# Optimization experiments

Hardware: AMD Instinct MI355X
Metric: run time of the kernel (lower is better)

The kernel has to match this reference:

```python
import math
import jax, jax.numpy as jnp
import numpy as np

HEAD = 8
D_HEAD = 32
D_MODEL = 256
N = 20000
E_LOCAL = 80000
E_BOND = 60000
E_GLOBAL = 400000
MAX_DEG = 32
MAX_DIST = 64


def segment_softmax(x, seg, num_segments):
    # softmax over entries sharing the same segment id (scatter_softmax)
    m = jax.ops.segment_max(x, seg, num_segments=num_segments)
    e = jnp.exp(x - m[seg])
    s = jax.ops.segment_sum(e, seg, num_segments=num_segments)
    return e / s[seg]


def setup_inputs() -> dict:
    key = jax.random.key(0)
    ks = jax.random.split(key, 16)
    s_in = 1.0 / math.sqrt(D_MODEL)
    s_out = 1.0 / math.sqrt(2 * D_MODEL)
    dist_emb = jax.random.normal(ks[7], (MAX_DIST + 1, D_MODEL), jnp.float32) * 0.02
    dist_emb = dist_emb.at[MAX_DIST].set(0.0)  # padding_idx
    return {
        "f_node": jax.random.normal(ks[0], (N, D_MODEL), jnp.float32),
        "f_bond": jax.random.normal(ks[1], (E_BOND, D_MODEL), jnp.float32),
        "deg_matrix": jax.random.randint(ks[2], (N,), 0, MAX_DEG + 1),
        "dist_matrix": jax.random.randint(ks[3], (E_GLOBAL,), 0, MAX_DIST + 1),
        "bond_idx": jax.random.randint(ks[4], (2, E_LOCAL), 0, N),
        "query_idx": jax.random.randint(ks[5], (E_GLOBAL,), 0, N),
        "key_idx": jax.random.randint(ks[6], (E_GLOBAL,), 0, N),
        "attention_bond_idx": jnp.arange(E_BOND),
        "deg_emb": jax.random.normal(ks[8], (MAX_DEG + 1, D_MODEL), jnp.float32) * 0.02,
        "dist_emb": dist_emb,
        "Wq_w": jax.random.normal(ks[9], (D_MODEL, 2 * D_MODEL), jnp.float32) * s_in,
        "Wq_b": jnp.zeros((2 * D_MODEL,), jnp.float32),
        "Wk_w": jax.random.normal(ks[10], (D_MODEL, 2 * D_MODEL), jnp.float32) * s_in,
        "Wk_b": jnp.zeros((2 * D_MODEL,), jnp.float32),
        "Wv_w": jax.random.normal(ks[11], (D_MODEL, 2 * D_MODEL), jnp.float32) * s_in,
        "Wv_b": jnp.zeros((2 * D_MODEL,), jnp.float32),
        "out_w": jax.random.normal(ks[12], (2 * D_MODEL, D_MODEL), jnp.float32) * s_out,
        "out_b": jnp.zeros((D_MODEL,), jnp.float32),
        "bond_emb_w": jax.random.normal(ks[13], (D_MODEL, 2 * D_MODEL), jnp.float32) * s_in,
        "bond_emb_b": jnp.zeros((2 * D_MODEL,), jnp.float32),
        "bond_update_w": jax.random.normal(ks[14], (2 * D_MODEL, D_MODEL), jnp.float32) * s_out,
        "bond_update_b": jnp.zeros((D_MODEL,), jnp.float32),
    }


def reference(f_node, f_bond, deg_matrix, dist_matrix, bond_idx, query_idx, key_idx,
              attention_bond_idx, deg_emb, dist_emb, Wq_w, Wq_b, Wk_w, Wk_b, Wv_w, Wv_b,
              out_w, out_b, bond_emb_w, bond_emb_b, bond_update_w, bond_update_b):
    scale = 1.0 / math.sqrt(D_HEAD)
    n = f_node.shape[0]
    e_bond = f_bond.shape[0]

    f_deg = deg_emb[deg_matrix].reshape(n, HEAD, D_HEAD)                  # [N,H,Dh]
    ab_vb = f_bond @ bond_emb_w + bond_emb_b                               # [Eb,2D]
    attention_bond, value_bond = jnp.split(ab_vb, 2, axis=-1)
    attention_bond = attention_bond.reshape(e_bond, HEAD, D_HEAD)
    value_bond = value_bond.reshape(e_bond, HEAD, D_HEAD)
    f_dist = dist_emb[dist_matrix].reshape(-1, HEAD, D_HEAD)               # [Eg,H,Dh]

    q = (f_node @ Wq_w + Wq_b).reshape(n, 2 * HEAD, D_HEAD)
    k = (f_node @ Wk_w + Wk_b).reshape(n, 2 * HEAD, D_HEAD)
    v = (f_node @ Wv_w + Wv_b).reshape(n, 2 * HEAD, D_HEAD)
    q_local, q_global = q[:, :HEAD], q[:, HEAD:]
    k_local, k_global = k[:, :HEAD], k[:, HEAD:]
    v_local, v_global = v[:, :HEAD], v[:, HEAD:]

    src, dst = bond_idx[0], bond_idx[1]
    # ---- local (bond) attention ----
    score_local = q_local[dst] * k_local[src]                              # [El,H,Dh]
    score_local = score_local.at[:e_bond].add(attention_bond)
    score_local = score_local.sum(-1) * scale                              # [El,H]
    score_local = segment_softmax(score_local, dst, n)
    local_out = v_local[src].at[:e_bond].add(value_bond)
    local_out = local_out * score_local[:, :, None]
    local_out = jax.ops.segment_sum(local_out, dst, num_segments=n)
    local_out = local_out.reshape(n, HEAD * D_HEAD)

    # ---- global (distance) attention ----
    kg = k_global + f_deg
    score_global = q_global[query_idx] * kg[key_idx]                       # [Eg,H,Dh]
    score_global = score_global.at[attention_bond_idx].add(attention_bond)
    score_global = (score_global + f_dist).sum(-1) * scale                 # [Eg,H]
    score_global = segment_softmax(score_global, query_idx, n)
    global_out = v_global[key_idx] * score_global[:, :, None]
    global_out = jax.ops.segment_sum(global_out, query_idx, num_segments=n)
    global_out = global_out.reshape(n, HEAD * D_HEAD)

    out = jnp.concatenate([local_out, global_out], axis=-1) @ out_w + out_b  # [N,D]
    bond_out = jnp.concatenate([f_bond, out[src[:e_bond]]], axis=-1)
    bond_out = bond_out @ bond_update_w + bond_update_b                      # [Eb,D]
    return out, bond_out
```

## Files before the change

### kernel.cpp

```cpp
#include <hip/hip_runtime.h>
#include <math.h>

typedef unsigned short u16;
typedef unsigned int u32;
typedef __attribute__((ext_vector_type(8))) short s16x8;
typedef __attribute__((ext_vector_type(4))) unsigned short u16x4;
typedef __attribute__((ext_vector_type(4))) float f32x4;

__device__ __forceinline__ float bf2f(u16 x) { return __uint_as_float(((u32)x) << 16); }
__device__ __forceinline__ u16 f2bf(float f) {
    u32 u = __float_as_uint(f);
    u32 r = u + 0x7fffu + ((u >> 16) & 1u);
    return (u16)(r >> 16);
}

__device__ __forceinline__ void gll16(const u16* g, u16* l) {
    __builtin_amdgcn_global_load_lds((const __attribute__((address_space(1))) void*)g,
                                     (__attribute__((address_space(3))) void*)l,
                                     16, 0, 0);
}

template <int MODE>
__global__ __launch_bounds__(256) void gemm128(
    const u16* __restrict__ Abf, const u16* __restrict__ A2b,
    const u16* __restrict__ BT, const float* __restrict__ bias,
    u16* __restrict__ Cb, float* __restrict__ Cf, u16* __restrict__ C2b,
    const float* __restrict__ auxemb, const int* __restrict__ auxidx,
    float* __restrict__ absum, int M, int N, int K)
{
    __shared__ u16 lsmem[2 * 16384];

    const int tid = threadIdx.x;
    const int wave = tid >> 6;
    const int lane = tid & 63;
    const int l15 = lane & 15;
    const int quad = lane >> 4;
    const int wr = wave >> 1, wc = wave & 1;

    const int gx = gridDim.x;
    const int nwg = gx * gridDim.y;
    int flat = blockIdx.y * gx + blockIdx.x;
    {
        const int q = nwg >> 3, r8 = nwg & 7;
        const int xcd = flat & 7, loc = flat >> 3;
        flat = (xcd < r8 ? xcd * (q + 1) : r8 * (q + 1) + (xcd - r8) * q) + loc;
    }
    const int tileRow = (flat / gx) * 128;
    const int tileCol = (flat % gx) * 128;

    const int srow = tid >> 3;
    const int ks = ((tid & 7) ^ (srow & 7)) * 8;

    const u16 *gA[4], *gB[4], *gA2[4];
#pragma unroll
    for (int j = 0; j < 4; j++) {
        const int ra = j * 32 + srow;
        const int pa = (MODE == 3) ? 256 : K;
        gA[j] = Abf + (size_t)(tileRow + ra) * pa + ks;
        gB[j] = BT + (size_t)(tileCol + ra) * K + ks;
        if (MODE == 3)
            gA2[j] = A2b + (size_t)auxidx[min(tileRow + ra, M - 1)] * 256 + ks;
        else
            gA2[j] = nullptr;
    }

#define STAGE(TK, BUF)                                                         \
    {                                                                          \
        u16* lb_ = lsmem + (BUF)*16384;                                        \
        const int kk_ = (TK)*64;                                               \
        _Pragma("unroll")                                                      \
        for (int j = 0; j < 4; j++) {                                          \
            const u16* sa;                                                     \
            if (MODE == 3) sa = (kk_ < 256) ? gA[j] + kk_ : gA2[j] + (kk_ - 256); \
            else sa = gA[j] + kk_;                                             \
            gll16(sa, lb_ + j * 2048 + tid * 8);                               \
            gll16(gB[j] + kk_, lb_ + 8192 + j * 2048 + tid * 8);               \
        }                                                                      \
    }

    f32x4 acc[4][4] = {};
    const int nt = K >> 6;

    STAGE(0, 0);
    STAGE(1, 1);

    for (int t = 0; t < nt; ++t) {
        if (t + 2 < nt) asm volatile("s_waitcnt vmcnt(8)" ::: "memory");
        else            asm volatile("s_waitcnt vmcnt(0)" ::: "memory");
        __builtin_amdgcn_s_barrier();
        __builtin_amdgcn_sched_barrier(0);

        const u16* lb = lsmem + (t & 1) * 16384;
#pragma unroll
        for (int kh = 0; kh < 2; kh++) {
            const int xk = ((quad + 4 * kh) ^ (l15 & 7)) * 8;
            s16x8 a[4], b[4];
#pragma unroll
            for (int mi = 0; mi < 4; mi++)
                a[mi] = *(const s16x8*)(lb + (wr * 64 + mi * 16 + l15) * 64 + xk);
#pragma unroll
            for (int ni = 0; ni < 4; ni++)
                b[ni] = *(const s16x8*)(lb + 8192 + (wc * 64 + ni * 16 + l15) * 64 + xk);
#pragma unroll
            for (int mi = 0; mi < 4; mi++)
#pragma unroll
                for (int ni = 0; ni < 4; ni++)
                    acc[mi][ni] = __builtin_amdgcn_mfma_f32_16x16x32_bf16(
                        a[mi], b[ni], acc[mi][ni], 0, 0, 0);
        }

        __builtin_amdgcn_sched_barrier(0);
        asm volatile("s_waitcnt lgkmcnt(0)" ::: "memory");
        __builtin_amdgcn_s_barrier();
        __builtin_amdgcn_sched_barrier(0);
        if (t + 2 < nt) STAGE(t + 2, t & 1);
    }
#undef STAGE

#pragma unroll
    for (int mi = 0; mi < 4; mi++) {
#pragma unroll
        for (int i = 0; i < 4; i++) {
            const int r = tileRow + wr * 64 + mi * 16 + quad * 4 + i;
            const bool rok = (r < M);
#pragma unroll
            for (int ni = 0; ni < 4; ni++) {
                const int c = tileCol + wc * 64 + ni * 16 + l15;
                float v = acc[mi][ni][i] + bias[c];
                if (MODE == 2) {
                    if (tileCol < 256) {
                        float s = v;
                        s += __shfl_xor(s, 1, 16);
                        s += __shfl_xor(s, 2, 16);
                        s += __shfl_xor(s, 4, 16);
                        s += __shfl_xor(s, 8, 16);
                        if (rok && l15 == 0) atomicAdd(&absum[r * 8 + (c >> 5)], s);
                    } else {
                        if (rok) Cb[(size_t)r * 256 + (c - 256)] = f2bf(v);
                    }
                } else if (MODE == 3) {
                    if (rok) Cf[(size_t)r * N + c] = v;
                } else if (MODE == 4) {
                    if (rok) {
                        Cf[(size_t)r * N + c] = v;
                        C2b[(size_t)r * N + c] = f2bf(v);
                    }
                } else {
                    const int which = c >> 9;
                    const int cc = c & 511;
                    if (which == 1 && cc >= 256)
                        v += auxemb[(size_t)auxidx[min(r, M - 1)] * 256 + (cc - 256)];
                    if (rok) Cb[((size_t)which * M + r) * 512 + cc] = f2bf(v);
                }
            }
        }
    }
}

__global__ __launch_bounds__(256) void prep_k(
    const float* __restrict__ Wq_w, const float* __restrict__ Wk_w,
    const float* __restrict__ Wv_w, const float* __restrict__ be_w,
    const float* __restrict__ out_w, const float* __restrict__ bu_w,
    u16* __restrict__ wT,
    const float* __restrict__ Wq_b, const float* __restrict__ Wk_b,
    const float* __restrict__ Wv_b, float* __restrict__ biasC,
    const float* __restrict__ dist_emb, float* __restrict__ distsum)
{
    const int b = blockIdx.x;
    if (b < 3072) {
        const int idx6 = b >> 9;
        const int r = ((b & 511) << 8) + threadIdx.x;
        const float* s = (idx6 == 0) ? Wq_w : (idx6 == 1) ? Wk_w
                       : (idx6 == 2) ? Wv_w : (idx6 == 3) ? be_w
                       : (idx6 == 4) ? out_w : bu_w;
        u16* dst = wT + (size_t)idx6 * 131072;
        if (idx6 < 4) {
            const int n = r >> 8, k = r & 255;
            dst[r] = f2bf(s[(size_t)k * 512 + n]);
        } else {
            const int n = r >> 9, k = r & 511;
            dst[r] = f2bf(s[(size_t)k * 256 + n]);
        }
    } else {
        const int u = (b - 3072) * 256 + threadIdx.x;
        if (u < 512) biasC[u] = Wq_b[u];
        else if (u < 1024) biasC[u] = Wk_b[u - 512];
        else if (u < 1536) biasC[u] = Wv_b[u - 1024];
        else if (u < 1536 + 520) {
            const float* p = dist_emb + (size_t)(u - 1536) * 32;
            float sm = 0.f;
#pragma unroll
            for (int j = 0; j < 32; j++) sm += p[j];
            distsum[u - 1536] = sm;
        }
    }
}

__global__ __launch_bounds__(256) void cvt2_k(
    const float* __restrict__ f_node, const float* __restrict__ f_bond,
    u16* __restrict__ fnb, u16* __restrict__ fbb,
    int N_, int MPN, int EB, int MPB)
{
    const int t = blockIdx.x * 256 + threadIdx.x;
    const int q1 = MPN * 64;
    const int q2 = MPB * 64;
    if (t < q1) {
        const int r = t >> 6;
        f32x4 v = {0.f, 0.f, 0.f, 0.f};
        if (r < N_) v = *(const f32x4*)(f_node + (size_t)t * 4);
        u16x4 o;
#pragma unroll
        for (int j = 0; j < 4; j++) o[j] = f2bf(v[j]);
        *(u16x4*)(fnb + (size_t)t * 4) = o;
    } else if (t < q1 + q2) {
        const int u = t - q1;
        const int r = u >> 6;
        f32x4 v = {0.f, 0.f, 0.f, 0.f};
        if (r < EB) v = *(const f32x4*)(f_bond + (size_t)u * 4);
        u16x4 o;
#pragma unroll
        for (int j = 0; j < 4; j++) o[j] = f2bf(v[j]);
        *(u16x4*)(fbb + (size_t)u * 4) = o;
    }
}

__global__ __launch_bounds__(256) void hist2_k(const int* __restrict__ bdst,
                                               const int* __restrict__ qidx,
                                               int* __restrict__ cnt,
                                               int N_, int EL, int EG)
{
    const int e = blockIdx.x * 256 + threadIdx.x;
    if (e < EL) atomicAdd(&cnt[bdst[e]], 1);
    else if (e < EL + EG) atomicAdd(&cnt[N_ + qidx[e - EL]], 1);
}

__global__ __launch_bounds__(1024) void scan2_k(
    const int* __restrict__ cnt_l, int* __restrict__ offs_l, int* __restrict__ cur_l,
    const int* __restrict__ cnt_g, int* __restrict__ offs_g, int* __restrict__ cur_g,
    int n)
{
    const int* cnt = blockIdx.x ? cnt_g : cnt_l;
    int* offs = blockIdx.x ? offs_g : offs_l;
    int* cursor = blockIdx.x ? cur_g : cur_l;
    __shared__ int part[1024];
    const int tid = threadIdx.x;
    const int per = (n + 1023) / 1024;
    int local[32];
    int s = 0;
    for (int j = 0; j < per; j++) {
        int idx = tid * per + j;
        int c = (idx < n) ? cnt[idx] : 0;
        local[j] = s;
        s += c;
    }
    part[tid] = s;
    __syncthreads();
    for (int st = 1; st < 1024; st <<= 1) {
        int v = (tid >= st) ? part[tid - st] : 0;
        __syncthreads();
        part[tid] += v;
        __syncthreads();
    }
    int pre = (tid == 0) ? 0 : part[tid - 1];
    for (int j = 0; j < per; j++) {
        int idx = tid * per + j;
        if (idx < n) { int o = pre + local[j]; offs[idx] = o; cursor[idx] = o; }
    }
    if (tid == 1023) offs[n] = part[1023];
}

__global__ __launch_bounds__(256) void scatter2_k(
    const int* __restrict__ bdst, const int* __restrict__ qidx,
    int* __restrict__ cur_l, int* __restrict__ cur_g,
    int* __restrict__ list_l, int* __restrict__ list_g, int EL, int EG)
{
    const int e = blockIdx.x * 256 + threadIdx.x;
    if (e < EL) {
        int pos = atomicAdd(&cur_l[bdst[e]], 1);
        list_l[pos] = e;
    } else if (e < EL + EG) {
        const int e2 = e - EL;
        int pos = atomicAdd(&cur_g[qidx[e2]], 1);
        list_g[pos] = e2;
    }
}

template <bool GLOB>
__device__ __forceinline__ void attn_half(
    const u16* __restrict__ qb, const u16* __restrict__ kb,
    const u16* __restrict__ vbuf, const u16* __restrict__ vb,
    const int* __restrict__ offs, const int* __restrict__ lst,
    const int* __restrict__ oth, const int* __restrict__ dist,
    const float* __restrict__ absum, const float* __restrict__ distsum,
    u16* __restrict__ out, int node, int EB, float scale)
{
    const int lane = threadIdx.x & 63;
    const int head = lane >> 3;
    const int cbase = (GLOB ? 256 : 0) + lane * 4;

    const u16x4 qv = *(const u16x4*)(qb + (size_t)node * 512 + cbase);
    const float q0 = bf2f(qv[0]), q1 = bf2f(qv[1]), q2 = bf2f(qv[2]), q3 = bf2f(qv[3]);

    const int s0 = offs[node], s1 = offs[node + 1];
    float a0 = 0.f, a1 = 0.f, a2 = 0.f, a3 = 0.f, den = 0.f;
    const u16x4 zv = {0, 0, 0, 0};

#define LOADS(S, IDX)                                                          \
    {                                                                          \
        e##S = __shfl(e_l, (IDX));                                             \
        const int src = __shfl(src_l, (IDX));                                  \
        kv##S = *(const u16x4*)(kb + (size_t)src * 512 + cbase);               \
        vv##S = *(const u16x4*)(vbuf + (size_t)src * 512 + cbase);             \
        ab##S = (e##S < EB) ? absum[e##S * 8 + head] : 0.f;                    \
        if (GLOB) {                                                            \
            const int d = __shfl(d_l, (IDX));                                  \
            ds##S = distsum[d * 8 + head];                                     \
        }                                                                      \
        if (!GLOB)                                                             \
            wv##S = (e##S < EB) ? *(const u16x4*)(vb + (size_t)e##S * 256 +    \
                                                  lane * 4)                    \
                                : zv;                                          \
    }

#define COMP(S)                                                                \
    {                                                                          \
        float t = q0 * bf2f(kv##S[0]) + q1 * bf2f(kv##S[1]) +                  \
                  q2 * bf2f(kv##S[2]) + q3 * bf2f(kv##S[3]);                   \
        t += __shfl_xor(t, 1);                                                 \
        t += __shfl_xor(t, 2);                                                 \
        t += __shfl_xor(t, 4);                                                 \
        t += ab##S;                                                            \
        if (GLOB) t += ds##S;                                                  \
        const float p = __expf(t * scale);                                     \
        den += p;                                                              \
        float v0 = bf2f(vv##S[0]), v1 = bf2f(vv##S[1]);                        \
        float v2 = bf2f(vv##S[2]), v3 = bf2f(vv##S[3]);                        \
        if (!GLOB) {                                                           \
            v0 += bf2f(wv##S[0]); v1 += bf2f(wv##S[1]);                        \
            v2 += bf2f(wv##S[2]); v3 += bf2f(wv##S[3]);                        \
        }                                                                      \
        a0 += p * v0; a1 += p * v1; a2 += p * v2; a3 += p * v3;                \
    }

    for (int base = s0; base < s1; base += 64) {
        const int cnt = min(64, s1 - base);
        const int gi = base + lane;
        int e_l = 0, src_l = 0, d_l = 0;
        if (gi < s1) {
            e_l = lst[gi];
            src_l = oth[e_l];
            if (GLOB) d_l = dist[e_l];
        }

        int eX, eY;
        u16x4 kvX, vvX, wvX = zv, kvY, vvY, wvY = zv;
        float abX, dsX = 0.f, abY, dsY = 0.f;

        LOADS(X, 0);
        int i = 0;
        for (; i + 2 <= cnt; i += 2) {
            LOADS(Y, i + 1);
            COMP(X);
            if (i + 2 < cnt) LOADS(X, i + 2);
            COMP(Y);
        }
        if (i < cnt) COMP(X);
    }
#undef LOADS
#undef COMP

    const float inv = (den > 0.f) ? 1.f / den : 0.f;
    u16x4 o;
    o[0] = f2bf(a0 * inv); o[1] = f2bf(a1 * inv);
    o[2] = f2bf(a2 * inv); o[3] = f2bf(a3 * inv);
    *(u16x4*)(out + (size_t)node * 512 + cbase) = o;
}

__global__ __launch_bounds__(256) void attn_fused(
    const u16* __restrict__ qb, const u16* __restrict__ kb,
    const u16* __restrict__ vbuf, const u16* __restrict__ vb,
    const int* __restrict__ offs_l, const int* __restrict__ list_l,
    const int* __restrict__ bsrc,
    const int* __restrict__ offs_g, const int* __restrict__ list_g,
    const int* __restrict__ kidx,
    const int* __restrict__ dist, const float* __restrict__ absum,
    const float* __restrict__ distsum, u16* __restrict__ out,
    int Nn, int EB, float scale)
{
    const int w = blockIdx.x * 4 + (threadIdx.x >> 6);
    if (w >= 2 * Nn) return;
    if (w < Nn)
        attn_half<false>(qb, kb, vbuf, vb, offs_l, list_l, bsrc, dist, absum,
                         distsum, out, w, EB, scale);
    else
        attn_half<true>(qb, kb, vbuf, vb, offs_g, list_g, kidx, dist, absum,
                        distsum, out, w - Nn, EB, scale);
}

extern "C" void kernel_launch(void* const* d_in, const int* in_sizes, int n_in,
                              void* d_out, int out_size, void* d_ws, size_t ws_size,
                              hipStream_t stream)
{
    const float* f_node  = (const float*)d_in[0];
    const float* f_bond  = (const float*)d_in[1];
    const int* deg       = (const int*)d_in[2];
    const int* dist      = (const int*)d_in[3];
    const int* bond_idx  = (const int*)d_in[4];
    const int* qidx      = (const int*)d_in[5];
    const int* kidx      = (const int*)d_in[6];
    const float* deg_emb = (const float*)d_in[8];
    const float* dist_emb= (const float*)d_in[9];
    const float* Wq_w = (const float*)d_in[10]; const float* Wq_b = (const float*)d_in[11];
    const float* Wk_w = (const float*)d_in[12]; const float* Wk_b = (const float*)d_in[13];
    const float* Wv_w = (const float*)d_in[14]; const float* Wv_b = (const float*)d_in[15];
    const float* out_w = (const float*)d_in[16]; const float* out_b = (const float*)d_in[17];
    const float* be_w  = (const float*)d_in[18]; const float* be_b  = (const float*)d_in[19];
    const float* bu_w  = (const float*)d_in[20]; const float* bu_b  = (const float*)d_in[21];

    const int N_ = in_sizes[0] / 256;
    const int EB = in_sizes[1] / 256;
    const int EL = in_sizes[4] / 2;
    const int EG = in_sizes[5];
    const float scale = 0.17677669529663689f;

    const int MPN = ((N_ + 127) / 128) * 128;
    const int MPB = ((EB + 127) / 128) * 128;

    const int* bsrc = bond_idx;
    const int* bdst = bond_idx + EL;

    u16* qb   = (u16*)d_ws;
    u16* kb   = qb + (size_t)N_ * 512;
    u16* vbuf = kb + (size_t)N_ * 512;
    u16* vb   = vbuf + (size_t)N_ * 512;
    u16* wT   = vb + (size_t)EB * 256;
    u16* wqT = wT;
    u16* beT = wT + 3 * 131072;
    u16* owT = wT + 4 * 131072;
    u16* buT = wT + 5 * 131072;
    float* distsum  = (float*)(wT + 6 * 131072);
    float* biasC    = distsum + 1024;
    u16* attn_out = (u16*)(biasC + 1536);
    u16* fnb      = attn_out;
    u16* fbb      = attn_out + (size_t)MPN * 512;
    u16* outb     = fbb + (size_t)MPB * 256;
    float* absum    = (float*)(outb + (size_t)N_ * 256);
    int*   cnt_l    = (int*)(absum + (size_t)EB * 8);
    int*   cnt_g    = cnt_l + N_;
    size_t zbytes   = ((size_t)EB * 8 + 2 * (size_t)N_) * 4;
    int*   offs_l   = cnt_g + N_;
    int*   offs_g   = offs_l + N_ + 4;
    int*   cur_l    = offs_g + N_ + 4;
    int*   cur_g    = cur_l + N_;
    int*   list_l   = cur_g + N_;
    int*   list_g   = list_l + EL;

    float* outp  = (float*)d_out;
    float* bondp = outp + (size_t)N_ * 256;

    hipMemsetAsync((void*)absum, 0, zbytes, stream);

    prep_k<<<3072 + 9, 256, 0, stream>>>(Wq_w, Wk_w, Wv_w, be_w, out_w, bu_w,
                                         wT, Wq_b, Wk_b, Wv_b, biasC,
                                         dist_emb, distsum);

    cvt2_k<<<(MPN * 64 + MPB * 64 + 255) / 256, 256, 0, stream>>>(
        f_node, f_bond, fnb, fbb, N_, MPN, EB, MPB);

    hist2_k<<<(EL + EG + 255) / 256, 256, 0, stream>>>(bdst, qidx, cnt_l, N_, EL, EG);
    scan2_k<<<2, 1024, 0, stream>>>(cnt_l, offs_l, cur_l, cnt_g, offs_g, cur_g, N_);
    scatter2_k<<<(EL + EG + 255) / 256, 256, 0, stream>>>(bdst, qidx, cur_l, cur_g,
                                                          list_l, list_g, EL, EG);

    dim3 g5(12, MPN / 128);
    gemm128<5><<<g5, 256, 0, stream>>>(fnb, nullptr, wqT, biasC, qb, nullptr, nullptr, deg_emb, deg, nullptr, N_, 1536, 256);

    dim3 gb(4, MPB / 128);
    gemm128<2><<<gb, 256, 0, stream>>>(fbb, nullptr, beT, be_b, vb, nullptr, nullptr, nullptr, nullptr, absum, EB, 512, 256);

    attn_fused<<<(2 * N_ + 3) / 4, 256, 0, stream>>>(qb, kb, vbuf, vb,
        offs_l, list_l, bsrc, offs_g, list_g, kidx, dist, absum, distsum,
        attn_out, N_, EB, scale);

    dim3 go(2, MPN / 128);
    gemm128<4><<<go, 256, 0, stream>>>(attn_out, nullptr, owT, out_b, nullptr, outp, outb, nullptr, nullptr, nullptr, N_, 256, 512);

    dim3 gu(2, MPB / 128);
    gemm128<3><<<gu, 256, 0, stream>>>(fbb, outb, buT, bu_b, nullptr, bondp, nullptr, nullptr, bsrc, nullptr, EB, 256, 512);
}
```

Baseline: 539.7 us.

## Give each wave private LDS tiles to remove workgroup barriers in GEMM

Each of the four waves now loads its own 64-row A and B slices into a private LDS region, so the main loop drops both s_barrier calls and only waits on its own vmcnt/lgkmcnt. The K step per stage shrinks from 64 to 32 with a new XOR swizzle matching the narrower rows. The cost is duplicated global traffic: A rows are loaded by two waves and B rows by two waves. There are also twice as many loop iterations and less latency hiding per stage.

```diff
diff --git a/kernel.cpp b/kernel.cpp
--- a/kernel.cpp
+++ b/kernel.cpp
@@ -28,7 +28,7 @@
     const float* __restrict__ auxemb, const int* __restrict__ auxidx,
     float* __restrict__ absum, int M, int N, int K)
 {
-    __shared__ u16 lsmem[2 * 16384];
+    __shared__ u16 lsmem[4 * 8192];
 
     const int tid = threadIdx.x;
     const int wave = tid >> 6;
@@ -36,6 +36,7 @@
     const int l15 = lane & 15;
     const int quad = lane >> 4;
     const int wr = wave >> 1, wc = wave & 1;
+    const int wb = wave * 8192;
 
     const int gx = gridDim.x;
     const int nwg = gx * gridDim.y;
@@ -48,72 +49,70 @@
     const int tileRow = (flat / gx) * 128;
     const int tileCol = (flat % gx) * 128;
 
-    const int srow = tid >> 3;
-    const int ks = ((tid & 7) ^ (srow & 7)) * 8;
+    const int srow = lane >> 2;
+    const int csrc8 = ((lane & 3) ^ ((lane >> 3) & 3)) * 8;
 
     const u16 *gA[4], *gB[4], *gA2[4];
 #pragma unroll
     for (int j = 0; j < 4; j++) {
-        const int ra = j * 32 + srow;
+        const int rowA = tileRow + wr * 64 + j * 16 + srow;
+        const int rowB = tileCol + wc * 64 + j * 16 + srow;
         const int pa = (MODE == 3) ? 256 : K;
-        gA[j] = Abf + (size_t)(tileRow + ra) * pa + ks;
-        gB[j] = BT + (size_t)(tileCol + ra) * K + ks;
+        gA[j] = Abf + (size_t)rowA * pa + csrc8;
+        gB[j] = BT + (size_t)rowB * K + csrc8;
         if (MODE == 3)
-            gA2[j] = A2b + (size_t)auxidx[min(tileRow + ra, M - 1)] * 256 + ks;
+            gA2[j] = A2b + (size_t)auxidx[min(rowA, M - 1)] * 256 + csrc8;
         else
             gA2[j] = nullptr;
     }
+    const int lane8 = lane * 8;
 
 #define STAGE(TK, BUF)                                                         \
     {                                                                          \
-        u16* lb_ = lsmem + (BUF)*16384;                                        \
-        const int kk_ = (TK)*64;                                               \
+        u16* lb_ = lsmem + wb + (BUF)*4096;                                    \
+        const int kk_ = (TK)*32;                                               \
         _Pragma("unroll")                                                      \
         for (int j = 0; j < 4; j++) {                                          \
             const u16* sa;                                                     \
             if (MODE == 3) sa = (kk_ < 256) ? gA[j] + kk_ : gA2[j] + (kk_ - 256); \
             else sa = gA[j] + kk_;                                             \
-            gll16(sa, lb_ + j * 2048 + tid * 8);                               \
-            gll16(gB[j] + kk_, lb_ + 8192 + j * 2048 + tid * 8);               \
+            gll16(sa, lb_ + j * 512 + lane8);                                  \
+            gll16(gB[j] + kk_, lb_ + 2048 + j * 512 + lane8);                  \
         }                                                                      \
     }
 
     f32x4 acc[4][4] = {};
-    const int nt = K >> 6;
+    const int nt = K >> 5;
 
     STAGE(0, 0);
     STAGE(1, 1);
 
+    const int xq8 = (quad ^ ((l15 >> 1) & 3)) * 8;
+
     for (int t = 0; t < nt; ++t) {
-        if (t + 2 < nt) asm volatile("s_waitcnt vmcnt(8)" ::: "memory");
+        if (t + 1 < nt) asm volatile("s_waitcnt vmcnt(8)" ::: "memory");
         else            asm volatile("s_waitcnt vmcnt(0)" ::: "memory");
-        __builtin_amdgcn_s_barrier();
-        __builtin_amdgcn_sched_barrier(0);
-
-        const u16* lb = lsmem + (t & 1) * 16384;
-#pragma unroll
-        for (int kh = 0; kh < 2; kh++) {
-            const int xk = ((quad + 4 * kh) ^ (l15 & 7)) * 8;
-            s16x8 a[4], b[4];
-#pragma unroll
-            for (int mi = 0; mi < 4; mi++)
-                a[mi] = *(const s16x8*)(lb + (wr * 64 + mi * 16 + l15) * 64 + xk);
+
+        const u16* lbA = lsmem + wb + (t & 1) * 4096;
+        const u16* lbB = lbA + 2048;
+        s16x8 a[4], b[4];
+#pragma unroll
+        for (int mi = 0; mi < 4; mi++)
+            a[mi] = *(const s16x8*)(lbA + (mi * 16 + l15) * 32 + xq8);
+#pragma unroll
+        for (int ni = 0; ni < 4; ni++)
+            b[ni] = *(const s16x8*)(lbB + (ni * 16 + l15) * 32 + xq8);
+#pragma unroll
+        for (int mi = 0; mi < 4; mi++)
 #pragma unroll
             for (int ni = 0; ni < 4; ni++)
-                b[ni] = *(const s16x8*)(lb + 8192 + (wc * 64 + ni * 16 + l15) * 64 + xk);
-#pragma unroll
-            for (int mi = 0; mi < 4; mi++)
-#pragma unroll
-                for (int ni = 0; ni < 4; ni++)
-                    acc[mi][ni] = __builtin_amdgcn_mfma_f32_16x16x32_bf16(
-                        a[mi], b[ni], acc[mi][ni], 0, 0, 0);
-        }
-
-        __builtin_amdgcn_sched_barrier(0);
-        asm volatile("s_waitcnt lgkmcnt(0)" ::: "memory");
-        __builtin_amdgcn_s_barrier();
-        __builtin_amdgcn_sched_barrier(0);
-        if (t + 2 < nt) STAGE(t + 2, t & 1);
+                acc[mi][ni] = __builtin_amdgcn_mfma_f32_16x16x32_bf16(
+                    a[mi], b[ni], acc[mi][ni], 0, 0, 0);
+
+        if (t + 2 < nt) {
+            asm volatile("s_waitcnt lgkmcnt(0)" ::: "memory");
+            STAGE(t + 2, t & 1);
+        }
     }
 #undef STAGE
 
```

After: 559.4 us. 3.6% more time.
